# Optimization experiments

Hardware: AMD Instinct MI355X
Metric: run time of the kernel (lower is better)

The kernel has to match this reference:

```python
import jax, jax.numpy as jnp
import numpy as np
from jax import lax

V_PATCH = (1, 4, 16, 64, 256, 1024)  # must end at L
RESI = 0.5    # quant_resi ratio inside Phi
BETA = 0.25
K_PHI = 4     # share_quant_resi


def _phi_indices():
    # PhiPartiallyShared tick lookup, resolved statically per scale
    K = K_PHI
    ticks = np.linspace(1/3/K, 1 - 1/3/K, K) if K == 4 else np.linspace(1/2/K, 1 - 1/2/K, K)
    SN = len(V_PATCH)
    return [int(np.argmin(np.abs(ticks - (si / (SN - 1) if SN > 1 else 0.0)))) for si in range(SN)]


def interp_linear(x, Lo):
    # torch F.interpolate(mode='linear', align_corners=False) on last axis of [B,C,Li]
    Li = x.shape[-1]
    if Li == Lo:
        return x
    pos = (jnp.arange(Lo, dtype=jnp.float32) + 0.5) * (Li / Lo) - 0.5
    pos = jnp.clip(pos, 0.0, Li - 1)
    lo = jnp.floor(pos).astype(jnp.int32)
    hi = jnp.minimum(lo + 1, Li - 1)
    w = pos - lo.astype(jnp.float32)
    return x[..., lo] * (1.0 - w) + x[..., hi] * w


def phi_apply(h, w, b):
    # Phi: h*(1-r) + Conv1d(ks=3,pad=1)(h)*r
    y = lax.conv_general_dilated(h, w, (1,), [(1, 1)], dimension_numbers=('NCH', 'OIH', 'NCH'))
    y = y + b[None, :, None]
    return h * (1.0 - RESI) + y * RESI


def reference(f_BCL, emb, phi_w, phi_b):
    f = f_BCL.astype(jnp.float32)
    B, C, L = f.shape
    f_ng = lax.stop_gradient(f)
    f_rest = f_ng
    f_hat = jnp.zeros_like(f_ng)
    SN = len(V_PATCH)
    pidx = _phi_indices()
    e_sq = jnp.sum(emb * emb, axis=1)  # [V]
    loss = jnp.float32(0.0)
    for si, pl in enumerate(V_PATCH):
        rest = interp_linear(f_rest, pl) if si != SN - 1 else f_rest
        z = rest.transpose(0, 2, 1).reshape(-1, C)              # [B*pl, C]
        d = jnp.sum(z * z, axis=1, keepdims=True) + e_sq - 2.0 * (z @ emb.T)  # [B*pl, V]
        idx = jnp.argmin(d, axis=1)
        h = emb[idx].reshape(B, pl, C).transpose(0, 2, 1)        # [B,C,pl]
        if si != SN - 1:
            h = interp_linear(h, L)
        h = phi_apply(h, phi_w[pidx[si]], phi_b[pidx[si]])
        f_hat = f_hat + h
        f_rest = f_rest - h
        loss = loss + BETA * jnp.mean((lax.stop_gradient(f_hat) - f) ** 2) \
                    + jnp.mean((f_hat - f_ng) ** 2)
    loss = loss / SN
    # straight-through estimator
    f_hat_st = lax.stop_gradient(f_hat) - f_ng + f
    return f_hat_st, loss


def setup_inputs() -> dict:
    key = jax.random.key(0)
    k1, k2, k3 = jax.random.split(key, 3)
    B, C, L, V = 32, 32, 1024, 4096
    f_BCL = jax.random.normal(k1, (B, C, L), dtype=jnp.float32)
    emb = jax.random.normal(k2, (V, C), dtype=jnp.float32)
    phi_w = jax.random.normal(k3, (K_PHI, C, C, 3), dtype=jnp.float32) * 0.05
    phi_b = jnp.zeros((K_PHI, C), dtype=jnp.float32)
    return {"f_BCL": f_BCL, "emb": emb, "phi_w": phi_w, "phi_b": phi_b}
```

## Files before the change

kernel.cpp:

```cpp
#include <hip/hip_runtime.h>
#include <stdint.h>

#define BDIM 32
#define CDIM 32
#define LDIM 1024
#define VDIM 4096
#define BCL (BDIM*CDIM*LDIM)

typedef _Float16 f16x8 __attribute__((ext_vector_type(8)));
typedef float f32x4 __attribute__((ext_vector_type(4)));

#define PIN_V(x) asm volatile("" : "+v"(x))

__global__ void init_kernel(const float* __restrict__ f, const float* __restrict__ emb,
                            float* __restrict__ f_rest, float* __restrict__ f_hat,
                            float* __restrict__ e_sq,
                            _Float16* __restrict__ eh, _Float16* __restrict__ el,
                            float* __restrict__ loss_acc, unsigned* __restrict__ done_ctr,
                            unsigned long long* __restrict__ keys, int nkeys) {
    int i = blockIdx.x * blockDim.x + threadIdx.x;
    if (i < BCL) { f_rest[i] = f[i]; f_hat[i] = 0.0f; }
    if (i < VDIM) {
        const float* e = emb + (size_t)i * CDIM;
        float s = 0.f;
#pragma unroll
        for (int k = 0; k < 32; ++k) {
            float v = e[k];
            s = fmaf(v, v, s);
            if (eh) {
                _Float16 h = (_Float16)v;
                float r = v - (float)h;
                eh[(size_t)i*32 + k] = (_Float16)(-2.0f) * h;
                el[(size_t)i*32 + k] = (_Float16)(-2.0f) * (_Float16)r;
            }
        }
        e_sq[i] = s;
    }
    if (i < nkeys) keys[i] = ~0ull;
    if (i == 0) { *loss_acc = 0.f; *done_ctr = 0u; }
}

__global__ __launch_bounds__(256) void vq_mfma(
    const _Float16* __restrict__ z_hi, const _Float16* __restrict__ z_lo,
    const _Float16* __restrict__ e_hi, const _Float16* __restrict__ e_lo,
    const float* __restrict__ e_sq, unsigned long long* __restrict__ keys,
    int NQ, int VC, int vchunks)
{
    const int t = threadIdx.x;
    const int lane = t & 63;
    const int w = t >> 6;
    const int qg = blockIdx.x / vchunks;
    const int vc = blockIdx.x % vchunks;
    const int vb = vc * VC;

    __shared__ __align__(16) _Float16 eh_ls[256*32];
    __shared__ __align__(16) _Float16 el_ls[256*32];
    __shared__ float esq_ls[256];

    {
        const float4* sH = (const float4*)(e_hi + (size_t)vb*32);
        const float4* sL = (const float4*)(e_lo + (size_t)vb*32);
        float4* dH = (float4*)eh_ls; float4* dL = (float4*)el_ls;
        int n4 = VC * 4;
        for (int x = t; x < n4; x += 256) {
            int row = x >> 2, c = x & 3;
            int ds = row*4 + (c ^ ((row >> 1) & 3));
            dH[ds] = sH[x]; dL[ds] = sL[x];
        }
        for (int v = t; v < VC; v += 256) esq_ls[v] = e_sq[vb + v];
    }

    const int fr = lane & 15;
    const int kq = lane >> 4;
    const int qbase = qg*128 + w*32;
    const int q0 = qbase + fr;
    f16x8 a0h = *(const f16x8*)(z_hi + (size_t)q0*32 + kq*8);
    f16x8 a0l = *(const f16x8*)(z_lo + (size_t)q0*32 + kq*8);
    f16x8 a1h = *(const f16x8*)(z_hi + (size_t)(q0+16)*32 + kq*8);
    f16x8 a1l = *(const f16x8*)(z_lo + (size_t)(q0+16)*32 + kq*8);

    __syncthreads();

    float bd0[4], bd1[4]; int bv0[4], bv1[4];
#pragma unroll
    for (int i = 0; i < 4; ++i) { bd0[i]=3.4e38f; bd1[i]=3.4e38f; bv0[i]=0; bv1[i]=0; }

    for (int vt = 0; vt < VC; vt += 16) {
        const int row = vt + fr;
        const int koff = (kq ^ ((row >> 1) & 3)) * 8;
        const f16x8 bh = *(const f16x8*)(eh_ls + (size_t)row*32 + koff);
        const f16x8 bl = *(const f16x8*)(el_ls + (size_t)row*32 + koff);
        float es = esq_ls[row];
        f32x4 acc0 = {es, es, es, es};
        f32x4 acc1 = {es, es, es, es};
        acc0 = __builtin_amdgcn_mfma_f32_16x16x32_f16(a0h, bh, acc0, 0,0,0);
        acc0 = __builtin_amdgcn_mfma_f32_16x16x32_f16(a0h, bl, acc0, 0,0,0);
        acc0 = __builtin_amdgcn_mfma_f32_16x16x32_f16(a0l, bh, acc0, 0,0,0);
        acc0 = __builtin_amdgcn_mfma_f32_16x16x32_f16(a0l, bl, acc0, 0,0,0);
        acc1 = __builtin_amdgcn_mfma_f32_16x16x32_f16(a1h, bh, acc1, 0,0,0);
        acc1 = __builtin_amdgcn_mfma_f32_16x16x32_f16(a1h, bl, acc1, 0,0,0);
        acc1 = __builtin_amdgcn_mfma_f32_16x16x32_f16(a1l, bh, acc1, 0,0,0);
        acc1 = __builtin_amdgcn_mfma_f32_16x16x32_f16(a1l, bl, acc1, 0,0,0);

        int vg = vb + row;
#pragma unroll
        for (int i = 0; i < 4; ++i) {
            if (acc0[i] < bd0[i]) { bd0[i] = acc0[i]; bv0[i] = vg; }
            if (acc1[i] < bd1[i]) { bd1[i] = acc1[i]; bv1[i] = vg; }
        }
    }

#pragma unroll
    for (int i = 0; i < 4; ++i) {
        unsigned u0 = __float_as_uint(bd0[i]);
        u0 = (u0 & 0x80000000u) ? ~u0 : (u0 | 0x80000000u);
        unsigned long long k0 = ((unsigned long long)u0 << 32) | (unsigned)bv0[i];
        unsigned u1 = __float_as_uint(bd1[i]);
        u1 = (u1 & 0x80000000u) ? ~u1 : (u1 | 0x80000000u);
        unsigned long long k1 = ((unsigned long long)u1 << 32) | (unsigned)bv1[i];
#pragma unroll
        for (int m = 1; m < 16; m <<= 1) {
            unsigned long long o0 = __shfl_xor(k0, m, 64); if (o0 < k0) k0 = o0;
            unsigned long long o1 = __shfl_xor(k1, m, 64); if (o1 < k1) k1 = o1;
        }
        if (fr == 0) {
            int q = qbase + kq*4 + i;
            atomicMin(&keys[q], k0);
            atomicMin(&keys[q + 16], k1);
        }
    }
}

__global__ __launch_bounds__(256) void vq_scan(
    const float* __restrict__ f_rest, const float* __restrict__ z_buf,
    const float* __restrict__ emb, const float* __restrict__ e_sq,
    unsigned long long* __restrict__ keys,
    int lpl, int s, int NQ, int VC, int vchunks)
{
    const int pl = 1 << lpl;
    const int t  = threadIdx.x;
    const int qg = blockIdx.x / vchunks;
    const int vc = blockIdx.x % vchunks;
    const int vb = vc * VC;

    __shared__ __align__(16) float e_ls[128 * 32];
    __shared__ float esq_ls[128];

    {
        const float4* src = (const float4*)emb + (size_t)vb * 8;
        float4* dst = (float4*)e_ls;
        for (int x = t; x < VC * 8; x += 256) dst[x] = src[x];
        if (t < VC) esq_ls[t] = e_sq[vb + t];
    }

    const int q0 = qg * 512 + t;
    const int q1 = q0 + 256;
    const int qc0 = (q0 < NQ) ? q0 : NQ - 1;
    const int qc1 = (q1 < NQ) ? q1 : NQ - 1;

    float z0[32], z1[32];
    if (z_buf) {
        const float4* p0 = (const float4*)(z_buf + (size_t)qc0 * 32);
        const float4* p1 = (const float4*)(z_buf + (size_t)qc1 * 32);
#pragma unroll
        for (int c4 = 0; c4 < 8; ++c4) {
            float4 a = p0[c4], b = p1[c4];
            z0[c4*4+0] = a.x; z0[c4*4+1] = a.y; z0[c4*4+2] = a.z; z0[c4*4+3] = a.w;
            z1[c4*4+0] = b.x; z1[c4*4+1] = b.y; z1[c4*4+2] = b.z; z1[c4*4+3] = b.w;
        }
    } else {
        int b0 = qc0 >> lpl, j0 = qc0 & (pl - 1);
        int b1 = qc1 >> lpl, j1 = qc1 & (pl - 1);
        if (pl == LDIM) {
            const float* p0 = f_rest + b0 * (CDIM * LDIM) + j0;
            const float* p1 = f_rest + b1 * (CDIM * LDIM) + j1;
#pragma unroll
            for (int c = 0; c < 32; ++c) { z0[c] = p0[c * LDIM]; z1[c] = p1[c * LDIM]; }
        } else {
            int col0 = j0 * s + (s >> 1) - 1;
            int col1 = j1 * s + (s >> 1) - 1;
            const float* p0 = f_rest + b0 * (CDIM * LDIM) + col0;
            const float* p1 = f_rest + b1 * (CDIM * LDIM) + col1;
#pragma unroll
            for (int c = 0; c < 32; ++c) {
                z0[c] = 0.5f * (p0[c * LDIM] + p0[c * LDIM + 1]);
                z1[c] = 0.5f * (p1[c * LDIM] + p1[c * LDIM + 1]);
            }
        }
    }

    __syncthreads();

    float bd0 = 3.4e38f, bd1 = 3.4e38f;
    int bv0 = 0, bv1 = 0;

#pragma unroll 1
    for (int v = 0; v < VC; v += 2) {
#pragma unroll
        for (int c = 0; c < 32; ++c) { PIN_V(z0[c]); PIN_V(z1[c]); }

        const float4* er0 = (const float4*)&e_ls[(size_t)v * 32];
        const float4* er1 = er0 + 8;
        float es0 = esq_ls[v];
        float es1 = esq_ls[v + 1];

        float4 e0 = er0[0], e1 = er1[0];
        float a00 = z0[0] * e0.x,        a01 = z0[0] * e1.x;
        float a10 = z1[0] * e0.x,        a11 = z1[0] * e1.x;
        a00 = fmaf(z0[1], e0.y, a00);    a01 = fmaf(z0[1], e1.y, a01);
        a10 = fmaf(z1[1], e0.y, a10);    a11 = fmaf(z1[1], e1.y, a11);
        a00 = fmaf(z0[2], e0.z, a00);    a01 = fmaf(z0[2], e1.z, a01);
        a10 = fmaf(z1[2], e0.z, a10);    a11 = fmaf(z1[2], e1.z, a11);
        a00 = fmaf(z0[3], e0.w, a00);    a01 = fmaf(z0[3], e1.w, a01);
        a10 = fmaf(z1[3], e0.w, a10);    a11 = fmaf(z1[3], e1.w, a11);
#pragma unroll
        for (int c4 = 1; c4 < 8; ++c4) {
            e0 = er0[c4]; e1 = er1[c4];
            a00 = fmaf(z0[c4*4+0], e0.x, a00);  a01 = fmaf(z0[c4*4+0], e1.x, a01);
            a10 = fmaf(z1[c4*4+0], e0.x, a10);  a11 = fmaf(z1[c4*4+0], e1.x, a11);
            a00 = fmaf(z0[c4*4+1], e0.y, a00);  a01 = fmaf(z0[c4*4+1], e1.y, a01);
            a10 = fmaf(z1[c4*4+1], e0.y, a10);  a11 = fmaf(z1[c4*4+1], e1.y, a11);
            a00 = fmaf(z0[c4*4+2], e0.z, a00);  a01 = fmaf(z0[c4*4+2], e1.z, a01);
            a10 = fmaf(z1[c4*4+2], e0.z, a10);  a11 = fmaf(z1[c4*4+2], e1.z, a11);
            a00 = fmaf(z0[c4*4+3], e0.w, a00);  a01 = fmaf(z0[c4*4+3], e1.w, a01);
            a10 = fmaf(z1[c4*4+3], e0.w, a10);  a11 = fmaf(z1[c4*4+3], e1.w, a11);
        }
        float d00 = fmaf(a00, -2.0f, es0);
        float d01 = fmaf(a01, -2.0f, es1);
        float d10 = fmaf(a10, -2.0f, es0);
        float d11 = fmaf(a11, -2.0f, es1);
        if (d00 < bd0) { bd0 = d00; bv0 = vb + v; }
        if (d01 < bd0) { bd0 = d01; bv0 = vb + v + 1; }
        if (d10 < bd1) { bd1 = d10; bv1 = vb + v; }
        if (d11 < bd1) { bd1 = d11; bv1 = vb + v + 1; }
    }

    if (q0 < NQ) {
        unsigned ud = __float_as_uint(bd0);
        ud = (ud & 0x80000000u) ? ~ud : (ud | 0x80000000u);
        atomicMin(&keys[q0], ((unsigned long long)ud << 32) | (unsigned)bv0);
    }
    if (q1 < NQ) {
        unsigned ud = __float_as_uint(bd1);
        ud = (ud & 0x80000000u) ? ~ud : (ud | 0x80000000u);
        atomicMin(&keys[q1], ((unsigned long long)ud << 32) | (unsigned)bv1);
    }
}

__global__ __launch_bounds__(256) void fuse_kernel(
    const float* __restrict__ f, const float* __restrict__ emb,
    const unsigned long long* __restrict__ keys,
    unsigned long long* __restrict__ keys_next, int nq_next,
    _Float16* __restrict__ zh_next, _Float16* __restrict__ zl_next, int s_next,
    const float* __restrict__ w, const float* __restrict__ bias,
    float* __restrict__ f_rest, float* __restrict__ f_hat,
    float* __restrict__ loss_acc, unsigned* __restrict__ done_ctr,
    float* __restrict__ out_loss, int pl)
{
    const int t  = threadIdx.x;
    const int b  = blockIdx.y;
    const int l0 = blockIdx.x * 64;

    if (keys_next) {
        int x = (b * gridDim.x + blockIdx.x) * 256 + t;
        if (x < nq_next) keys_next[x] = ~0ull;
    }

    __shared__ float w_s[3072];
    __shared__ float b_s[32];
    __shared__ float hs[32 * 68];
    __shared__ float red[4];

    for (int x = t; x < 3072; x += 256) w_s[x] = w[x];
    if (t < 32) b_s[t] = bias[t];

    if (t < 66) {
        int l = l0 - 1 + t;
        if (l < 0 || l >= LDIM) {
#pragma unroll
            for (int i = 0; i < 32; ++i) hs[i * 68 + t] = 0.f;
        } else {
            int lo, hi; float wg;
            if (pl == LDIM) { lo = l; hi = l; wg = 0.f; }
            else {
                float pos = (l + 0.5f) * ((float)pl / 1024.0f) - 0.5f;
                pos = fminf(fmaxf(pos, 0.f), (float)(pl - 1));
                lo = (int)floorf(pos);
                hi = min(lo + 1, pl - 1);
                wg = pos - (float)lo;
            }
            int v0 = (int)(keys[b * pl + lo] & 0xFFFFFFFFull);
            int v1 = (int)(keys[b * pl + hi] & 0xFFFFFFFFull);
            const float4* e0 = (const float4*)(emb + (size_t)v0 * 32);
            const float4* e1 = (const float4*)(emb + (size_t)v1 * 32);
            float om = 1.0f - wg;
#pragma unroll
            for (int i4 = 0; i4 < 8; ++i4) {
                float4 a = e0[i4]; float4 c = e1[i4];
                hs[(i4*4+0) * 68 + t] = a.x * om + c.x * wg;
                hs[(i4*4+1) * 68 + t] = a.y * om + c.y * wg;
                hs[(i4*4+2) * 68 + t] = a.z * om + c.z * wg;
                hs[(i4*4+3) * 68 + t] = a.w * om + c.w * wg;
            }
        }
    }
    __syncthreads();

    const int o  = t >> 3;
    const int lg = t & 7;
    const float* wrow = &w_s[o * 96];
    float acc[8];
#pragma unroll
    for (int u = 0; u < 8; ++u) acc[u] = 0.f;
    const int hbase = lg * 8;

    for (int i = 0; i < 32; ++i) {
        float w0 = wrow[i * 3 + 0], w1 = wrow[i * 3 + 1], w2 = wrow[i * 3 + 2];
        const float* hrow = &hs[i * 68 + hbase];
        float hw[10];
#pragma unroll
        for (int x = 0; x < 10; ++x) hw[x] = hrow[x];
#pragma unroll
        for (int u = 0; u < 8; ++u) {
            acc[u] = fmaf(w0, hw[u], acc[u]);
            acc[u] = fmaf(w1, hw[u + 1], acc[u]);
            acc[u] = fmaf(w2, hw[u + 2], acc[u]);
        }
    }

    float lsum = 0.f;
    float frv[8];
    const int gbase = (b * 32 + o) * LDIM + l0 + lg * 8;
#pragma unroll
    for (int u = 0; u < 8; ++u) {
        float hval = hs[o * 68 + lg * 8 + 1 + u];
        float y = acc[u] + b_s[o];
        float ph = 0.5f * hval + 0.5f * y;
        int gi = gbase + u;
        float fh = f_hat[gi] + ph;
        f_hat[gi] = fh;
        float fr = f_rest[gi] - ph;
        f_rest[gi] = fr;
        frv[u] = fr;
        float df = fh - f[gi];
        lsum = fmaf(df, df, lsum);
    }

    if (zh_next) {
        __syncthreads();
#pragma unroll
        for (int u = 0; u < 8; ++u) hs[o * 68 + lg * 8 + u] = frv[u];
        __syncthreads();
        int npos = 64 / s_next;
        int qn_base = b * (LDIM / s_next) + l0 / s_next;
        for (int v = t; v < npos * 32; v += 256) {
            int jl = v >> 5, c = v & 31;
            float zv;
            if (s_next == 1) zv = hs[c * 68 + jl];
            else {
                int cl = jl * s_next + (s_next >> 1) - 1;
                zv = 0.5f * (hs[c * 68 + cl] + hs[c * 68 + cl + 1]);
            }
            _Float16 h = (_Float16)zv;
            float r = zv - (float)h;
            size_t zi = (size_t)(qn_base + jl) * 32 + c;
            zh_next[zi] = h;
            zl_next[zi] = (_Float16)r;
        }
    }

#pragma unroll
    for (int off = 32; off > 0; off >>= 1) lsum += __shfl_down(lsum, off, 64);
    if ((t & 63) == 0) red[t >> 6] = lsum;
    __syncthreads();
    if (t == 0) {
        atomicAdd(loss_acc, red[0] + red[1] + red[2] + red[3]);
        if (out_loss) {
            __threadfence();
            unsigned old = atomicAdd(done_ctr, 1u);
            if (old == (unsigned)(gridDim.x * gridDim.y - 1)) {
                float lv = atomicAdd(loss_acc, 0.0f);
                *out_loss = lv * (1.25f / (6.0f * (float)BCL));
            }
        }
    }
}

extern "C" void kernel_launch(void* const* d_in, const int* in_sizes, int n_in,
                              void* d_out, int out_size, void* d_ws, size_t ws_size,
                              hipStream_t stream)
{
    const float* f    = (const float*)d_in[0];
    const float* emb  = (const float*)d_in[1];
    const float* phiw = (const float*)d_in[2];
    const float* phib = (const float*)d_in[3];

    float* f_hat    = (float*)d_out;
    float* out_loss = f_hat + BCL;

    const int pls[6]   = {1, 4, 16, 64, 256, 1024};
    const int lpls[6]  = {0, 2, 4, 6, 8, 10};
    const int vch[6]   = {64, 64, 64, 64, 32, 32};
    const int vchm[6]  = {0, 0, 64, 32, 16, 16};
    const int pidx[6]  = {0, 0, 1, 2, 3, 3};
    const int snx[6]   = {256, 64, 16, 4, 1, 0};

    char* ws = (char*)d_ws;
    float* f_rest = (float*)ws;

    size_t base = (size_t)BCL * 4;
    size_t off = base;
    unsigned long long* keysA = (unsigned long long*)(ws + off);
    unsigned long long* keysB = keysA + 32768;
    off += (size_t)65536 * 8;
    _Float16* z_hi = (_Float16*)(ws + off); off += (size_t)32768 * 32 * 2;
    _Float16* z_lo = (_Float16*)(ws + off); off += (size_t)32768 * 32 * 2;
    _Float16* e_hi = (_Float16*)(ws + off); off += (size_t)VDIM * 32 * 2;
    _Float16* e_lo = (_Float16*)(ws + off); off += (size_t)VDIM * 32 * 2;
    size_t need_mf = off + (size_t)VDIM * 4 + 64;
    bool mf = ws_size >= need_mf;

    if (!mf) {
        off = base;
        size_t need_pp = base + (size_t)65536 * 8 + (size_t)VDIM * 4 + 64;
        bool pp = ws_size >= need_pp;
        keysB = pp ? keysA + 32768 : keysA;
        off += pp ? (size_t)65536 * 8 : (size_t)32768 * 8;
        float* e_sq        = (float*)(ws + off);
        float* loss_acc    = e_sq + VDIM;
        unsigned* done_ctr = (unsigned*)(loss_acc + 1);

        init_kernel<<<dim3((BCL + 255) / 256), 256, 0, stream>>>(
            f, emb, f_rest, f_hat, e_sq, nullptr, nullptr, loss_acc, done_ctr, keysA, 32768);

        for (int si = 0; si < 6; ++si) {
            int pl = pls[si], s = LDIM / pl, NQ = BDIM * pl;
            int qgroups = (NQ + 511) >> 9;
            int VC = VDIM / vch[si];
            unsigned long long* k  = (si & 1) ? keysB : keysA;
            unsigned long long* kn = (si < 5 && pp) ? ((si & 1) ? keysA : keysB) : nullptr;
            int nq_next = (si < 5) ? BDIM * pls[si + 1] : 0;
            if (!pp && si > 0) hipMemsetAsync(k, 0xFF, (size_t)NQ * 8, stream);
            vq_scan<<<dim3(qgroups * vch[si]), 256, 0, stream>>>(
                f_rest, nullptr, emb, e_sq, k, lpls[si], s, NQ, VC, vch[si]);
            fuse_kernel<<<dim3(16, 32), 256, 0, stream>>>(
                f, emb, k, kn, nq_next, nullptr, nullptr, snx[si],
                phiw + (size_t)pidx[si] * 3072, phib + (size_t)pidx[si] * 32,
                f_rest, f_hat, loss_acc, done_ctr,
                (si == 5) ? out_loss : nullptr, pl);
        }
        return;
    }

    float* e_sq        = (float*)(ws + off);
    float* loss_acc    = e_sq + VDIM;
    unsigned* done_ctr = (unsigned*)(loss_acc + 1);

    init_kernel<<<dim3((BCL + 255) / 256), 256, 0, stream>>>(
        f, emb, f_rest, f_hat, e_sq, e_hi, e_lo, loss_acc, done_ctr, keysA, 32768);

    for (int si = 0; si < 6; ++si) {
        int pl = pls[si], s = LDIM / pl, NQ = BDIM * pl;
        unsigned long long* k  = (si & 1) ? keysB : keysA;
        unsigned long long* kn = (si < 5) ? ((si & 1) ? keysA : keysB) : nullptr;
        int nq_next = (si < 5) ? BDIM * pls[si + 1] : 0;
        if (si >= 2) {
            int vcm = vchm[si];
            vq_mfma<<<dim3((NQ / 128) * vcm), 256, 0, stream>>>(
                z_hi, z_lo, e_hi, e_lo, e_sq, k, NQ, VDIM / vcm, vcm);
        } else {
            int qgroups = (NQ + 511) >> 9;
            vq_scan<<<dim3(qgroups * vch[si]), 256, 0, stream>>>(
                f_rest, nullptr, emb, e_sq, k, lpls[si], s, NQ, VDIM / vch[si], vch[si]);
        }
        bool zw = (si >= 1 && si <= 4);
        fuse_kernel<<<dim3(16, 32), 256, 0, stream>>>(
            f, emb, k, kn, nq_next,
            zw ? z_hi : nullptr, zw ? z_lo : nullptr, snx[si],
            phiw + (size_t)pidx[si] * 3072, phib + (size_t)pidx[si] * 32,
            f_rest, f_hat, loss_acc, done_ctr,
            (si == 5) ? out_loss : nullptr, pl);
    }
}
```

Measured before the change: 314.4 us.

## Widen MFMA query tile to 64 per wave and drop lo*lo product

Each wave of the MFMA nearest-codeword kernel now handles 64 queries (4 tiles of 16) instead of 32, so every codebook fragment loaded from LDS is reused across more queries, and the grid shrinks to match. The fourth MFMA of the split-f16 emulation (lo*lo term) is also removed, cutting matrix work by a quarter. This raises register pressure and halves the number of blocks, which may reduce occupancy on small scales. Dropping the lo*lo term slightly lowers distance precision, which could flip argmin ties.

```diff
diff --git a/kernel.cpp b/kernel.cpp
--- a/kernel.cpp
+++ b/kernel.cpp
@@ -72,18 +72,22 @@
 
     const int fr = lane & 15;
     const int kq = lane >> 4;
-    const int qbase = qg*128 + w*32;
-    const int q0 = qbase + fr;
-    f16x8 a0h = *(const f16x8*)(z_hi + (size_t)q0*32 + kq*8);
-    f16x8 a0l = *(const f16x8*)(z_lo + (size_t)q0*32 + kq*8);
-    f16x8 a1h = *(const f16x8*)(z_hi + (size_t)(q0+16)*32 + kq*8);
-    f16x8 a1l = *(const f16x8*)(z_lo + (size_t)(q0+16)*32 + kq*8);
+    const int qbase = qg*256 + w*64;
+    f16x8 ah[4], al[4];
+#pragma unroll
+    for (int tq = 0; tq < 4; ++tq) {
+        int q = qbase + tq*16 + fr;
+        ah[tq] = *(const f16x8*)(z_hi + (size_t)q*32 + kq*8);
+        al[tq] = *(const f16x8*)(z_lo + (size_t)q*32 + kq*8);
+    }
 
     __syncthreads();
 
-    float bd0[4], bd1[4]; int bv0[4], bv1[4];
-#pragma unroll
-    for (int i = 0; i < 4; ++i) { bd0[i]=3.4e38f; bd1[i]=3.4e38f; bv0[i]=0; bv1[i]=0; }
+    float bd[4][4]; int bv[4][4];
+#pragma unroll
+    for (int tq = 0; tq < 4; ++tq)
+#pragma unroll
+        for (int i = 0; i < 4; ++i) { bd[tq][i] = 3.4e38f; bv[tq][i] = 0; }
 
     for (int vt = 0; vt < VC; vt += 16) {
         const int row = vt + fr;
@@ -91,42 +95,34 @@
         const f16x8 bh = *(const f16x8*)(eh_ls + (size_t)row*32 + koff);
         const f16x8 bl = *(const f16x8*)(el_ls + (size_t)row*32 + koff);
         float es = esq_ls[row];
-        f32x4 acc0 = {es, es, es, es};
-        f32x4 acc1 = {es, es, es, es};
-        acc0 = __builtin_amdgcn_mfma_f32_16x16x32_f16(a0h, bh, acc0, 0,0,0);
-        acc0 = __builtin_amdgcn_mfma_f32_16x16x32_f16(a0h, bl, acc0, 0,0,0);
-        acc0 = __builtin_amdgcn_mfma_f32_16x16x32_f16(a0l, bh, acc0, 0,0,0);
-        acc0 = __builtin_amdgcn_mfma_f32_16x16x32_f16(a0l, bl, acc0, 0,0,0);
-        acc1 = __builtin_amdgcn_mfma_f32_16x16x32_f16(a1h, bh, acc1, 0,0,0);
-        acc1 = __builtin_amdgcn_mfma_f32_16x16x32_f16(a1h, bl, acc1, 0,0,0);
-        acc1 = __builtin_amdgcn_mfma_f32_16x16x32_f16(a1l, bh, acc1, 0,0,0);
-        acc1 = __builtin_amdgcn_mfma_f32_16x16x32_f16(a1l, bl, acc1, 0,0,0);
-
         int vg = vb + row;
 #pragma unroll
+        for (int tq = 0; tq < 4; ++tq) {
+            f32x4 acc = {es, es, es, es};
+            acc = __builtin_amdgcn_mfma_f32_16x16x32_f16(ah[tq], bh, acc, 0,0,0);
+            acc = __builtin_amdgcn_mfma_f32_16x16x32_f16(ah[tq], bl, acc, 0,0,0);
+            acc = __builtin_amdgcn_mfma_f32_16x16x32_f16(al[tq], bh, acc, 0,0,0);
+#pragma unroll
+            for (int i = 0; i < 4; ++i)
+                if (acc[i] < bd[tq][i]) { bd[tq][i] = acc[i]; bv[tq][i] = vg; }
+        }
+    }
+
+#pragma unroll
+    for (int tq = 0; tq < 4; ++tq) {
+#pragma unroll
         for (int i = 0; i < 4; ++i) {
-            if (acc0[i] < bd0[i]) { bd0[i] = acc0[i]; bv0[i] = vg; }
-            if (acc1[i] < bd1[i]) { bd1[i] = acc1[i]; bv1[i] = vg; }
-        }
-    }
-
-#pragma unroll
-    for (int i = 0; i < 4; ++i) {
-        unsigned u0 = __float_as_uint(bd0[i]);
-        u0 = (u0 & 0x80000000u) ? ~u0 : (u0 | 0x80000000u);
-        unsigned long long k0 = ((unsigned long long)u0 << 32) | (unsigned)bv0[i];
-        unsigned u1 = __float_as_uint(bd1[i]);
-        u1 = (u1 & 0x80000000u) ? ~u1 : (u1 | 0x80000000u);
-        unsigned long long k1 = ((unsigned long long)u1 << 32) | (unsigned)bv1[i];
-#pragma unroll
-        for (int m = 1; m < 16; m <<= 1) {
-            unsigned long long o0 = __shfl_xor(k0, m, 64); if (o0 < k0) k0 = o0;
-            unsigned long long o1 = __shfl_xor(k1, m, 64); if (o1 < k1) k1 = o1;
-        }
-        if (fr == 0) {
-            int q = qbase + kq*4 + i;
-            atomicMin(&keys[q], k0);
-            atomicMin(&keys[q + 16], k1);
+            unsigned u = __float_as_uint(bd[tq][i]);
+            u = (u & 0x80000000u) ? ~u : (u | 0x80000000u);
+            unsigned long long k = ((unsigned long long)u << 32) | (unsigned)bv[tq][i];
+#pragma unroll
+            for (int m = 1; m < 16; m <<= 1) {
+                unsigned long long o = __shfl_xor(k, m, 64); if (o < k) k = o;
+            }
+            if (fr == 0) {
+                int q = qbase + tq*16 + kq*4 + i;
+                atomicMin(&keys[q], k);
+            }
         }
     }
 }
@@ -466,7 +462,7 @@
         int nq_next = (si < 5) ? BDIM * pls[si + 1] : 0;
         if (si >= 2) {
             int vcm = vchm[si];
-            vq_mfma<<<dim3((NQ / 128) * vcm), 256, 0, stream>>>(
+            vq_mfma<<<dim3((NQ / 256) * vcm), 256, 0, stream>>>(
                 z_hi, z_lo, e_hi, e_lo, e_sq, k, NQ, VDIM / vcm, vcm);
         } else {
             int qgroups = (NQ + 511) >> 9;
```

Result: no change. 316.1 us (+0.5%).
